# Kernel optimization log

Measured on AMD Instinct MI355X. Metric: run time of the kernel, lower is better.

## Reference

```python
import math
import jax, jax.numpy as jnp
import numpy as np

D_MODEL, N_STATE, SEQ_LEN = 1024, 64, 1024
DT_MIN, DT_MAX = 1e-3, 1e-1


def setup_inputs() -> dict:
    key = jax.random.key(0)
    kC, kdt = jax.random.split(key)
    A_real = -0.5 * jnp.ones((D_MODEL, N_STATE), jnp.float32)
    A_imag = math.pi * jnp.broadcast_to(
        jnp.arange(N_STATE, dtype=jnp.float32), (D_MODEL, N_STATE)
    )
    C = jax.random.normal(kC, (D_MODEL, N_STATE, 2), jnp.float32) * 0.5
    log_dt = (
        jax.random.uniform(kdt, (D_MODEL,), jnp.float32)
        * (math.log(DT_MAX) - math.log(DT_MIN))
        + math.log(DT_MIN)
    )
    B = jnp.ones((D_MODEL, N_STATE), jnp.float32)
    return {"A_real": A_real, "A_imag": A_imag, "C": C, "log_dt": log_dt,
            "B": B, "L": SEQ_LEN}


def reference(A_real, A_imag, C, log_dt, B, L):
    dt = jnp.exp(log_dt)                       # (d,)
    A = A_real + 1j * A_imag                   # (d,N) complex64
    dtA = A * dt[:, None]                      # (d,N)
    Cc = C[..., 0] + 1j * C[..., 1]            # (d,N) complex64
    ell = jnp.arange(L, dtype=jnp.float32)     # (L,)
    # A_bar ** l == exp(dtA * l): Vandermonde power expansion, (d,N,L)
    powers = jnp.exp(dtA[..., None] * ell)
    K = jnp.einsum('dn,dnl->dl', Cc * B.astype(Cc.dtype), powers)  # (d,L)
    return K.real * dt[:, None]
```

## Files before the change

### kernel.cpp

```cpp
#include <hip/hip_runtime.h>
#include <math.h>


#define D_MODEL 1024
#define N_STATE 64
#define SEQ_LEN 1024
#define CHUNK   8
#define TPD     128
#define NSPLIT  2
#define NPT     (N_STATE / NSPLIT)
#define BLOCK   (TPD * NSPLIT)

#define INV_2PI 0.15915494309189535

__device__ __forceinline__ float sin_rev(float f) { return __builtin_amdgcn_sinf(f); }
__device__ __forceinline__ float cos_rev(float f) { return __builtin_amdgcn_cosf(f); }

__global__ __launch_bounds__(BLOCK, 4) void s4d_kernel(
    const float* __restrict__ A_real, const float* __restrict__ A_imag,
    const float* __restrict__ C, const float* __restrict__ log_dt,
    const float* __restrict__ B, float* __restrict__ out)
{
  __shared__ float2 hiT[N_STATE][8];
  __shared__ float2 loT[N_STATE][16];
  __shared__ float4 ws[N_STATE];
  __shared__ float  red[CHUNK][TPD];

  const int tid = threadIdx.x;
  const int d   = blockIdx.x;
  const float dt = __expf(log_dt[d]);

  #pragma unroll
  for (int i = 0; i < 6; ++i) {
    const int e   = tid + BLOCK * i;
    const int n   = e / 24;
    const int idx = e - n * 24;
    const int steps = (idx < 8) ? (idx << 4) : (idx - 8);
    const float ar = A_real[d * N_STATE + n];
    const float ai = A_imag[d * N_STATE + n];
    const float xr = dt * ar;
    const double drev = (double)dt * (double)ai * INV_2PI;
    const double ph = drev * (double)steps;
    const float  fr = (float)(ph - floor(ph));
    const float mag = __expf(xr * (float)steps);
    const float2 v = make_float2(mag * cos_rev(fr), mag * sin_rev(fr));
    if (idx < 8) hiT[n][idx] = v; else loT[n][idx - 8] = v;
  }
  if (tid < N_STATE) {
    const int n = tid;
    const float ar = A_real[d * N_STATE + n];
    const float ai = A_imag[d * N_STATE + n];
    const float b  = B[d * N_STATE + n];
    const float cr = C[(d * N_STATE + n) * 2 + 0];
    const float ci = C[(d * N_STATE + n) * 2 + 1];
    const float xr = dt * ar;
    const double drev = (double)dt * (double)ai * INV_2PI;
    const double ph = drev * 128.0;
    const float  fr = (float)(ph - floor(ph));
    const float mag = __expf(xr * 128.0f);
    ws[n] = make_float4(cr * b * dt, ci * b * dt,
                        mag * cos_rev(fr), mag * sin_rev(fr));
  }
  __syncthreads();

  const int t     = tid & (TPD - 1);
  const int split = tid >> 7;
  const int thi   = t >> 4;
  const int tlo   = t & 15;

  float acc[CHUNK];
  #pragma unroll
  for (int j = 0; j < CHUNK; ++j) acc[j] = 0.0f;

  const int n0 = split * NPT;
  #pragma unroll 4
  for (int nn = 0; nn < NPT; ++nn) {
    const int n = n0 + nn;
    const float4 w4 = ws[n];
    const float2 h  = hiT[n][thi];
    const float2 l2 = loT[n][tlo];
    const float sr = fmaf(h.x, l2.x, -(h.y * l2.y));
    const float si = fmaf(h.x, l2.y,   h.y * l2.x);
    float u0 = fmaf(w4.x, sr, -(w4.y * si));
    const float yi = fmaf(w4.x, si, w4.y * sr);
    float u1 = fmaf(u0, w4.z, -(yi * w4.w));
    const float a2 = w4.z + w4.z;
    const float nb = -fmaf(w4.z, w4.z, w4.w * w4.w);
    acc[0] += u0;
    acc[1] += u1;
    #pragma unroll
    for (int j = 2; j < CHUNK; ++j) {
      const float u2 = fmaf(a2, u1, nb * u0);
      acc[j] += u2;
      u0 = u1; u1 = u2;
    }
  }

  if (split == 1) {
    #pragma unroll
    for (int j = 0; j < CHUNK; ++j) red[j][t] = acc[j];
  }
  __syncthreads();
  if (split == 0) {
    float* op = out + d * SEQ_LEN + t;
    #pragma unroll
    for (int j = 0; j < CHUNK; ++j) op[j * TPD] = acc[j] + red[j][t];
  }
}

extern "C" void kernel_launch(void* const* d_in, const int* in_sizes, int n_in,
                              void* d_out, int out_size, void* d_ws, size_t ws_size,
                              hipStream_t stream) {
  const float* A_real = (const float*)d_in[0];
  const float* A_imag = (const float*)d_in[1];
  const float* C      = (const float*)d_in[2];
  const float* log_dt = (const float*)d_in[3];
  const float* B      = (const float*)d_in[4];
  float* out = (float*)d_out;

  s4d_kernel<<<dim3(D_MODEL), dim3(BLOCK), 0, stream>>>(
      A_real, A_imag, C, log_dt, B, out);
}
```

Before: 72.36 us.

## Split state dimension eight ways with longer recurrence chunks and union LDS reduction

```diff
diff --git a/kernel.cpp b/kernel.cpp
--- a/kernel.cpp
+++ b/kernel.cpp
@@ -5,9 +5,9 @@
 #define D_MODEL 1024
 #define N_STATE 64
 #define SEQ_LEN 1024
-#define CHUNK   8
-#define TPD     128
-#define NSPLIT  2
+#define CHUNK   16
+#define TPD     64
+#define NSPLIT  8
 #define NPT     (N_STATE / NSPLIT)
 #define BLOCK   (TPD * NSPLIT)
 
@@ -16,35 +16,44 @@
 __device__ __forceinline__ float sin_rev(float f) { return __builtin_amdgcn_sinf(f); }
 __device__ __forceinline__ float cos_rev(float f) { return __builtin_amdgcn_cosf(f); }
 
-__global__ __launch_bounds__(BLOCK, 4) void s4d_kernel(
+union SMem {
+  struct {
+    float2 hiT[N_STATE][4];
+    float2 loT[N_STATE][16];
+    float4 wsA[N_STATE];
+    float2 wsB[N_STATE];
+  } tab;
+  float red[NSPLIT - 1][TPD][CHUNK];
+};
+
+__global__ __launch_bounds__(BLOCK, 8) void s4d_kernel(
     const float* __restrict__ A_real, const float* __restrict__ A_imag,
     const float* __restrict__ C, const float* __restrict__ log_dt,
     const float* __restrict__ B, float* __restrict__ out)
 {
-  __shared__ float2 hiT[N_STATE][8];
-  __shared__ float2 loT[N_STATE][16];
-  __shared__ float4 ws[N_STATE];
-  __shared__ float  red[CHUNK][TPD];
+  __shared__ SMem sm;
 
   const int tid = threadIdx.x;
   const int d   = blockIdx.x;
   const float dt = __expf(log_dt[d]);
 
   #pragma unroll
-  for (int i = 0; i < 6; ++i) {
-    const int e   = tid + BLOCK * i;
-    const int n   = e / 24;
-    const int idx = e - n * 24;
-    const int steps = (idx < 8) ? (idx << 4) : (idx - 8);
-    const float ar = A_real[d * N_STATE + n];
-    const float ai = A_imag[d * N_STATE + n];
-    const float xr = dt * ar;
-    const double drev = (double)dt * (double)ai * INV_2PI;
-    const double ph = drev * (double)steps;
-    const float  fr = (float)(ph - floor(ph));
-    const float mag = __expf(xr * (float)steps);
-    const float2 v = make_float2(mag * cos_rev(fr), mag * sin_rev(fr));
-    if (idx < 8) hiT[n][idx] = v; else loT[n][idx - 8] = v;
+  for (int i = 0; i < 3; ++i) {
+    const int e = tid + BLOCK * i;
+    if (e < N_STATE * 20) {
+      const int n   = e / 20;
+      const int idx = e - n * 20;
+      const int steps = (idx < 4) ? (idx << 4) : (idx - 4);
+      const float ar = A_real[d * N_STATE + n];
+      const float ai = A_imag[d * N_STATE + n];
+      const float xr = dt * ar;
+      const double drev = (double)dt * (double)ai * INV_2PI;
+      const double ph = drev * (double)steps;
+      const float  fr = (float)(ph - floor(ph));
+      const float mag = __expf(xr * (float)steps);
+      const float2 v = make_float2(mag * cos_rev(fr), mag * sin_rev(fr));
+      if (idx < 4) sm.tab.hiT[n][idx] = v; else sm.tab.loT[n][idx - 4] = v;
+    }
   }
   if (tid < N_STATE) {
     const int n = tid;
@@ -55,16 +64,18 @@
     const float ci = C[(d * N_STATE + n) * 2 + 1];
     const float xr = dt * ar;
     const double drev = (double)dt * (double)ai * INV_2PI;
-    const double ph = drev * 128.0;
+    const double ph = drev * (double)TPD;
     const float  fr = (float)(ph - floor(ph));
-    const float mag = __expf(xr * 128.0f);
-    ws[n] = make_float4(cr * b * dt, ci * b * dt,
-                        mag * cos_rev(fr), mag * sin_rev(fr));
+    const float mag = __expf(xr * (float)TPD);
+    const float str = mag * cos_rev(fr);
+    const float sti = mag * sin_rev(fr);
+    sm.tab.wsA[n] = make_float4(cr * b * dt, ci * b * dt, str, sti);
+    sm.tab.wsB[n] = make_float2(str + str, -(mag * mag));
   }
   __syncthreads();
 
   const int t     = tid & (TPD - 1);
-  const int split = tid >> 7;
+  const int split = tid >> 6;
   const int thi   = t >> 4;
   const int tlo   = t & 15;
 
@@ -73,38 +84,50 @@
   for (int j = 0; j < CHUNK; ++j) acc[j] = 0.0f;
 
   const int n0 = split * NPT;
-  #pragma unroll 4
+  #pragma unroll 2
   for (int nn = 0; nn < NPT; ++nn) {
     const int n = n0 + nn;
-    const float4 w4 = ws[n];
-    const float2 h  = hiT[n][thi];
-    const float2 l2 = loT[n][tlo];
+    const float4 w4 = sm.tab.wsA[n];
+    const float2 ab = sm.tab.wsB[n];
+    const float2 h  = sm.tab.hiT[n][thi];
+    const float2 l2 = sm.tab.loT[n][tlo];
     const float sr = fmaf(h.x, l2.x, -(h.y * l2.y));
     const float si = fmaf(h.x, l2.y,   h.y * l2.x);
     float u0 = fmaf(w4.x, sr, -(w4.y * si));
     const float yi = fmaf(w4.x, si, w4.y * sr);
     float u1 = fmaf(u0, w4.z, -(yi * w4.w));
-    const float a2 = w4.z + w4.z;
-    const float nb = -fmaf(w4.z, w4.z, w4.w * w4.w);
     acc[0] += u0;
     acc[1] += u1;
     #pragma unroll
     for (int j = 2; j < CHUNK; ++j) {
-      const float u2 = fmaf(a2, u1, nb * u0);
+      const float u2 = fmaf(ab.x, u1, ab.y * u0);
       acc[j] += u2;
       u0 = u1; u1 = u2;
     }
   }
 
-  if (split == 1) {
+  __syncthreads();
+  if (split != 0) {
+    float4* r4 = (float4*)sm.red[split - 1][t];
     #pragma unroll
-    for (int j = 0; j < CHUNK; ++j) red[j][t] = acc[j];
+    for (int q = 0; q < 4; ++q)
+      r4[q] = make_float4(acc[4*q], acc[4*q+1], acc[4*q+2], acc[4*q+3]);
   }
   __syncthreads();
   if (split == 0) {
+    #pragma unroll
+    for (int s = 0; s < NSPLIT - 1; ++s) {
+      const float4* r4 = (const float4*)sm.red[s][t];
+      #pragma unroll
+      for (int q = 0; q < 4; ++q) {
+        const float4 v = r4[q];
+        acc[4*q]   += v.x; acc[4*q+1] += v.y;
+        acc[4*q+2] += v.z; acc[4*q+3] += v.w;
+      }
+    }
     float* op = out + d * SEQ_LEN + t;
     #pragma unroll
-    for (int j = 0; j < CHUNK; ++j) op[j * TPD] = acc[j] + red[j][t];
+    for (int j = 0; j < CHUNK; ++j) op[j * TPD] = acc[j];
   }
 }
 
```

Result: no change. 72.61 us (+0.4%).
